# Performance work log

Hardware: AMD Instinct MI355X
Metric: run time of the kernel (lower is better)

## Reference

```python
import jax, jax.numpy as jnp
import numpy as np

NUM_HEADS = 8
TOP_K = 2
ROUTER_EPS = 1e-5
LN_EPS = 1e-5
ROPE_BASE = 10000.0


def _layernorm(x, g, b):
    m = x.mean(-1, keepdims=True)
    v = ((x - m) ** 2).mean(-1, keepdims=True)
    return (x - m) * jax.lax.rsqrt(v + LN_EPS) * g + b


def _rope_tables(frames, height, width, head_dim, dtype):
    # dim split per axis; head_dim divisible by 3 with even parts (96 -> 32/32/32)
    dpa = head_dim // 3

    def freqs(n, d):
        inv = 1.0 / (ROPE_BASE ** (jnp.arange(0, d, 2, dtype=jnp.float32) / d))
        f = jnp.outer(jnp.arange(n, dtype=jnp.float32), inv)
        return jnp.concatenate([f, f], axis=-1)  # [n, d]

    fx, fy, ft = freqs(width, dpa), freqs(height, dpa), freqs(frames, dpa)

    def grid(ax, ay, at):
        gx = jnp.broadcast_to(ax[None, None, :, :], (frames, height, width, dpa))
        gy = jnp.broadcast_to(ay[None, :, None, :], (frames, height, width, dpa))
        gt = jnp.broadcast_to(at[:, None, None, :], (frames, height, width, dpa))
        return jnp.concatenate([gx, gy, gt], -1).reshape(frames * height * width, 3 * dpa)

    cos = grid(jnp.cos(fx), jnp.cos(fy), jnp.cos(ft)).astype(dtype)
    sin = grid(jnp.sin(fx), jnp.sin(fy), jnp.sin(ft)).astype(dtype)
    return cos, sin


def _apply_rope(x, cos, sin):
    # x: [B, H, S, hd]; cos/sin: [S, hd] (broadcast over B, H)
    h = x.shape[-1] // 2
    rot = jnp.concatenate([-x[..., h:], x[..., :h]], axis=-1)
    return x * cos + rot * sin


def _expert(x, g, u, d):
    # SwiGLU expert: down(silu(gate(x)) * up(x))
    return (jax.nn.silu(x @ g) * (x @ u)) @ d


def _block(x, cos, sin, ln1_g, ln1_b, w_qkv, w_out, gate_w,
           eg, eu, ed, sg, su, sd, ln2_g, ln2_b):
    B, S, D = x.shape
    hd = D // NUM_HEADS
    # --- 3D-RoPE attention (pre-LN, non-causal) ---
    xn = _layernorm(x, ln1_g, ln1_b)
    qkv = (xn @ w_qkv).reshape(B, S, 3, NUM_HEADS, hd)
    q = jnp.moveaxis(qkv[:, :, 0], 1, 2)  # [B, H, S, hd]
    k = jnp.moveaxis(qkv[:, :, 1], 1, 2)
    v = jnp.moveaxis(qkv[:, :, 2], 1, 2)
    q = _apply_rope(q, cos, sin)
    k = _apply_rope(k, cos, sin)
    scores = jnp.einsum('bhqd,bhkd->bhqk', q, k) * (hd ** -0.5)
    attn = jax.nn.softmax(scores, axis=-1)
    o = jnp.einsum('bhqk,bhkd->bhqd', attn, v)
    o = jnp.moveaxis(o, 1, 2).reshape(B, S, D) @ w_out
    x = x + o
    # --- temporal MoE (top-k routing + shared expert) ---
    xf = x.reshape(-1, D)
    probs = jax.nn.softmax(xf @ gate_w, axis=-1)
    topv, topi = jax.lax.top_k(probs, TOP_K)
    topv = topv / (topv.sum(-1, keepdims=True) + ROUTER_EPS)
    E = eg.shape[0]
    # combine weight per (token, expert): sum over k slots routed to that expert
    comb = jnp.sum(topv[..., None] * (topi[..., None] == jnp.arange(E)), axis=1)  # [N, E]
    out = _expert(xf, sg, su, sd)  # shared expert on all tokens
    for e in range(E):
        out = out + comb[:, e:e + 1] * _expert(xf, eg[e], eu[e], ed[e])
    return _layernorm(x + out.reshape(B, S, D), ln2_g, ln2_b)


def setup_inputs() -> dict:
    key = jax.random.key(0)
    ks = jax.random.split(key, 10)
    B, S, D, F, E, L = 2, 2048, 768, 3072, 4, 2
    s = 0.02
    return {
        'x': jax.random.normal(ks[0], (B, S, D), jnp.float32),
        'height': 16, 'width': 16, 'frames': 8,
        'ln1_g': jnp.ones((L, D), jnp.float32),
        'ln1_b': jnp.zeros((L, D), jnp.float32),
        'w_qkv': jax.random.normal(ks[1], (L, D, 3 * D), jnp.float32) * s,
        'w_out': jax.random.normal(ks[2], (L, D, D), jnp.float32) * s,
        'gate_w': jax.random.normal(ks[3], (L, D, E), jnp.float32) * 0.01,
        'eg': jax.random.normal(ks[4], (L, E, D, F), jnp.float32) * s,
        'eu': jax.random.normal(ks[5], (L, E, D, F), jnp.float32) * s,
        'ed': jax.random.normal(ks[6], (L, E, F, D), jnp.float32) * s,
        'sg': jax.random.normal(ks[7], (L, D, F), jnp.float32) * s,
        'su': jax.random.normal(ks[8], (L, D, F), jnp.float32) * s,
        'sd': jax.random.normal(ks[9], (L, F, D), jnp.float32) * s,
        'ln2_g': jnp.ones((L, D), jnp.float32),
        'ln2_b': jnp.zeros((L, D), jnp.float32),
    }


def reference(x, height, width, frames, ln1_g, ln1_b, w_qkv, w_out, gate_w,
              eg, eu, ed, sg, su, sd, ln2_g, ln2_b):
    hd = x.shape[-1] // NUM_HEADS
    cos, sin = _rope_tables(frames, height, width, hd, x.dtype)
    for i in range(ln1_g.shape[0]):
        x = _block(x, cos, sin, ln1_g[i], ln1_b[i], w_qkv[i], w_out[i], gate_w[i],
                   eg[i], eu[i], ed[i], sg[i], su[i], sd[i], ln2_g[i], ln2_b[i])
    return x
```

## Files before the change

kernel.cpp:

```cpp
#include <hip/hip_runtime.h>
#include <stdint.h>

#define S_LEN 2048
#define DM    768
#define NHEAD 8
#define HDIM  96
#define HDP   128
#define FF    3072
#define FF2   6144
#define NEXP  4
#define NTOK  4096
#define NBH   16
#define HBROWS (2 * NTOK)

typedef unsigned short u16;
typedef short bf16x8 __attribute__((ext_vector_type(8)));
typedef float f32x4 __attribute__((ext_vector_type(4)));
typedef __attribute__((address_space(1))) void* gptr_t;
typedef __attribute__((address_space(3))) void* lptr_t;

__device__ __forceinline__ u16 f2bf(float f) {
  union { float f; uint32_t u; } v; v.f = f;
  uint32_t r = v.u + 0x7FFFu + ((v.u >> 16) & 1u);
  return (u16)(r >> 16);
}
__device__ __forceinline__ float bf2f(u16 h) {
  union { uint32_t u; float f; } v; v.u = ((uint32_t)h) << 16;
  return v.f;
}
__device__ __forceinline__ void split2(float f, u16& hi, u16& lo) {
  u16 h = f2bf(f);
  lo = f2bf(f - bf2f(h));
  hi = h;
}
__device__ __forceinline__ float siluf(float g) {
  return g / (1.0f + expf(-g));
}
__device__ __forceinline__ void gload16(const void* g, void* l) {
  __builtin_amdgcn_global_load_lds((gptr_t)(void*)g, (lptr_t)l, 16, 0, 0);
}

template<int MODE>
__global__ __launch_bounds__(256) void gemm_nt(
    const u16* __restrict__ A, const u16* __restrict__ B, void* __restrict__ Cv,
    int M, int N, int K, int lda, int ldb, long sA, long sB, long sC, int kspl,
    u16* __restrict__ hb)
{
  __shared__ u16 As[2][128 * 32];
  __shared__ u16 Bs[2][128 * 32];
  const int z = blockIdx.z;
  const int bh = z / kspl;
  const int kc = z - bh * kspl;
  const u16* Az = A + (long)bh * sA;
  const u16* Bz = B + (long)bh * sB;
  const int brow = blockIdx.y << 7;
  const int bcol = blockIdx.x << 7;
  const int tid = threadIdx.x;
  const int wid = tid >> 6;
  const int lane = tid & 63;
  const int wr = (wid >> 1) << 6;
  const int wc = (wid & 1) << 6;

  f32x4 acc[4][4] = {};
  const int a0 = (wid << 11) + (lane << 4);

  auto stage = [&](int buf, int k0) {
#pragma unroll
    for (int c = 0; c < 2; ++c) {
      int ab = a0 + (c << 10);
      int row = ab >> 6;
      int kcol = (ab & 63) >> 1;
      int ld = (wid << 11) + (c << 10);
      gload16(Az + (long)(brow + row) * lda + (k0 + kcol), (char*)As[buf] + ld);
      gload16(Bz + (long)(bcol + row) * ldb + (k0 + kcol), (char*)Bs[buf] + ld);
    }
  };

  const int kt = K / kspl;
  const int kbeg = kc * kt;
  const int nt = kt >> 5;
  stage(0, kbeg);
  __syncthreads();
  for (int t = 0; t < nt; ++t) {
    const int cur = t & 1;
    if (t + 1 < nt) stage(cur ^ 1, kbeg + ((t + 1) << 5));
    bf16x8 af[4], bfr[4];
    const int lr = lane & 15;
    const int lk = (lane >> 4) << 4;
#pragma unroll
    for (int m = 0; m < 4; ++m)
      af[m] = *(const bf16x8*)((const char*)As[cur] + (((wr + m * 16 + lr) << 6) + lk));
#pragma unroll
    for (int n = 0; n < 4; ++n)
      bfr[n] = *(const bf16x8*)((const char*)Bs[cur] + (((wc + n * 16 + lr) << 6) + lk));
#pragma unroll
    for (int m = 0; m < 4; ++m)
#pragma unroll
      for (int n = 0; n < 4; ++n)
        acc[m][n] = __builtin_amdgcn_mfma_f32_16x16x32_bf16(af[m], bfr[n], acc[m][n], 0, 0, 0);
    if (t + 1 < nt) __syncthreads();
  }

  const int crow0 = brow + wr + ((lane >> 4) << 2);
  const int ccol0 = bcol + wc + (lane & 15);
  const long cbase = (long)bh * sC;
  if constexpr (MODE == 5) {
    const int pbase = (bcol + wc) >> 5;
#pragma unroll
    for (int m = 0; m < 4; ++m)
#pragma unroll
      for (int np = 0; np < 2; ++np)
#pragma unroll
        for (int j = 0; j < 4; ++j) {
          int r = crow0 + m * 16 + j;
          float g = acc[m][2 * np][j], u = acc[m][2 * np + 1][j];
          int hcol = ((pbase + np) << 4) + (lane & 15);
          hb[(long)r * FF + hcol] = f2bf(siluf(g) * u);
        }
  } else {
#pragma unroll
    for (int m = 0; m < 4; ++m)
#pragma unroll
      for (int n = 0; n < 4; ++n)
#pragma unroll
        for (int j = 0; j < 4; ++j) {
          long idx = cbase + (long)(crow0 + m * 16 + j) * N + (ccol0 + n * 16);
          float v = acc[m][n][j];
          if constexpr (MODE == 2) ((u16*)Cv)[idx] = f2bf(v);
          else if constexpr (MODE == 3) unsafeAtomicAdd((float*)Cv + idx, v);
          else ((float*)Cv)[idx] = v;
        }
  }
}

template<int MODE>
__global__ __launch_bounds__(256) void gemm3_nt(
    const u16* __restrict__ Ah, const u16* __restrict__ Al,
    const u16* __restrict__ Bh, const u16* __restrict__ Bl,
    float* __restrict__ C,
    int M, int N, int K, int lda, int ldb, long sA, long sB, long sC, int kspl,
    u16* __restrict__ hbh, u16* __restrict__ hbl)
{
  __shared__ u16 Ash[2][128 * 32], Asl[2][128 * 32];
  __shared__ u16 Bsh[2][128 * 32], Bsl[2][128 * 32];
  const int z = blockIdx.z;
  const int bh = z / kspl;
  const int kc = z - bh * kspl;
  const u16* Azh = Ah + (long)bh * sA;
  const u16* Azl = Al + (long)bh * sA;
  const u16* Bzh = Bh + (long)bh * sB;
  const u16* Bzl = Bl + (long)bh * sB;
  const int brow = blockIdx.y << 7;
  const int bcol = blockIdx.x << 7;
  const int tid = threadIdx.x;
  const int wid = tid >> 6;
  const int lane = tid & 63;
  const int wr = (wid >> 1) << 6;
  const int wc = (wid & 1) << 6;

  f32x4 acc[4][4] = {};
  const int a0 = (wid << 11) + (lane << 4);

  auto stage = [&](int buf, int k0) {
#pragma unroll
    for (int c = 0; c < 2; ++c) {
      int ab = a0 + (c << 10);
      int row = ab >> 6;
      int kcol = (ab & 63) >> 1;
      long ao = (long)(brow + row) * lda + (k0 + kcol);
      long bo = (long)(bcol + row) * ldb + (k0 + kcol);
      int ld = (wid << 11) + (c << 10);
      gload16(Azh + ao, (char*)Ash[buf] + ld);
      gload16(Azl + ao, (char*)Asl[buf] + ld);
      gload16(Bzh + bo, (char*)Bsh[buf] + ld);
      gload16(Bzl + bo, (char*)Bsl[buf] + ld);
    }
  };

  const int kt = K / kspl;
  const int kbeg = kc * kt;
  const int nt = kt >> 5;
  stage(0, kbeg);
  __syncthreads();
  for (int t = 0; t < nt; ++t) {
    const int cur = t & 1;
    if (t + 1 < nt) stage(cur ^ 1, kbeg + ((t + 1) << 5));
    const int lr = lane & 15;
    const int lk = (lane >> 4) << 4;
    bf16x8 ah[4], al[4], bh_[4], bl[4];
#pragma unroll
    for (int m = 0; m < 4; ++m) {
      int off = ((wr + m * 16 + lr) << 6) + lk;
      ah[m] = *(const bf16x8*)((const char*)Ash[cur] + off);
      al[m] = *(const bf16x8*)((const char*)Asl[cur] + off);
    }
#pragma unroll
    for (int n = 0; n < 4; ++n) {
      int off = ((wc + n * 16 + lr) << 6) + lk;
      bh_[n] = *(const bf16x8*)((const char*)Bsh[cur] + off);
      bl[n] = *(const bf16x8*)((const char*)Bsl[cur] + off);
    }
#pragma unroll
    for (int m = 0; m < 4; ++m)
#pragma unroll
      for (int n = 0; n < 4; ++n) {
        acc[m][n] = __builtin_amdgcn_mfma_f32_16x16x32_bf16(al[m], bh_[n], acc[m][n], 0, 0, 0);
        acc[m][n] = __builtin_amdgcn_mfma_f32_16x16x32_bf16(ah[m], bl[n], acc[m][n], 0, 0, 0);
        acc[m][n] = __builtin_amdgcn_mfma_f32_16x16x32_bf16(ah[m], bh_[n], acc[m][n], 0, 0, 0);
      }
    if (t + 1 < nt) __syncthreads();
  }

  const int crow0 = brow + wr + ((lane >> 4) << 2);
  const int ccol0 = bcol + wc + (lane & 15);
  const long cbase = (long)bh * sC;
  if constexpr (MODE == 5) {
    const int pbase = (bcol + wc) >> 5;
#pragma unroll
    for (int m = 0; m < 4; ++m)
#pragma unroll
      for (int np = 0; np < 2; ++np)
#pragma unroll
        for (int j = 0; j < 4; ++j) {
          int r = crow0 + m * 16 + j;
          float g = acc[m][2 * np][j], u = acc[m][2 * np + 1][j];
          float h = siluf(g) * u;
          int hcol = ((pbase + np) << 4) + (lane & 15);
          u16 hh, ll; split2(h, hh, ll);
          hbh[(long)r * FF + hcol] = hh;
          hbl[(long)r * FF + hcol] = ll;
        }
  } else {
#pragma unroll
    for (int m = 0; m < 4; ++m)
#pragma unroll
      for (int n = 0; n < 4; ++n)
#pragma unroll
        for (int j = 0; j < 4; ++j) {
          long idx = cbase + (long)(crow0 + m * 16 + j) * N + (ccol0 + n * 16);
          if constexpr (MODE == 3) unsafeAtomicAdd(&C[idx], acc[m][n][j]);
          else C[idx] = acc[m][n][j];
        }
  }
}

template<int MODE>
__global__ __launch_bounds__(256) void gemm3i_nt(
    const u16* __restrict__ Ah, const u16* __restrict__ Al,
    const u16* __restrict__ Bh, const u16* __restrict__ Bl,
    float* __restrict__ C, int N, int K, int lda, int ldb, int ldc,
    const int* __restrict__ perm, const int* __restrict__ cnt,
    const int* __restrict__ cbase, int kspl, long wstride,
    u16* __restrict__ hbh, u16* __restrict__ hbl, const float* __restrict__ comb)
{
  const int z = blockIdx.z;
  const int e = z / kspl;
  const int kc = z - e * kspl;
  const int cn = cnt[e];
  const int brow = blockIdx.y << 7;
  if (brow >= cn) return;
  const int cb = cbase[e];
  const int* pe = perm + e * NTOK;
  const u16* Bhe = Bh + (long)e * wstride;
  const u16* Ble = Bl + (long)e * wstride;
  __shared__ u16 Ash[2][128 * 32], Asl[2][128 * 32];
  __shared__ u16 Bsh[2][128 * 32], Bsl[2][128 * 32];
  const int bcol = blockIdx.x << 7;
  const int tid = threadIdx.x;
  const int wid = tid >> 6;
  const int lane = tid & 63;
  const int wr = (wid >> 1) << 6;
  const int wc = (wid & 1) << 6;

  f32x4 acc[4][4] = {};
  const int a0 = (wid << 11) + (lane << 4);

  int arow[2];
#pragma unroll
  for (int c = 0; c < 2; ++c) {
    int ab = a0 + (c << 10);
    int row = ab >> 6;
    int g = brow + row;
    if constexpr (MODE == 5) {
      arow[c] = (g < cn) ? pe[g] : pe[brow];
    } else {
      arow[c] = cb + ((g < cn) ? g : (cn - 1));
    }
  }

  auto stage = [&](int buf, int k0) {
#pragma unroll
    for (int c = 0; c < 2; ++c) {
      int ab = a0 + (c << 10);
      int row = ab >> 6;
      int kcol = (ab & 63) >> 1;
      int ld = (wid << 11) + (c << 10);
      gload16(Ah + (long)arow[c] * lda + (k0 + kcol), (char*)Ash[buf] + ld);
      gload16(Al + (long)arow[c] * lda + (k0 + kcol), (char*)Asl[buf] + ld);
      long bo = (long)(bcol + row) * ldb + (k0 + kcol);
      gload16(Bhe + bo, (char*)Bsh[buf] + ld);
      gload16(Ble + bo, (char*)Bsl[buf] + ld);
    }
  };

  const int kt = K / kspl;
  const int kbeg = kc * kt;
  const int nt = kt >> 5;
  stage(0, kbeg);
  __syncthreads();
  for (int t = 0; t < nt; ++t) {
    const int cur = t & 1;
    if (t + 1 < nt) stage(cur ^ 1, kbeg + ((t + 1) << 5));
    const int lr = lane & 15;
    const int lk = (lane >> 4) << 4;
    bf16x8 ah[4], al[4], bh_[4], bl[4];
#pragma unroll
    for (int m = 0; m < 4; ++m) {
      int off = ((wr + m * 16 + lr) << 6) + lk;
      ah[m] = *(const bf16x8*)((const char*)Ash[cur] + off);
      al[m] = *(const bf16x8*)((const char*)Asl[cur] + off);
    }
#pragma unroll
    for (int n = 0; n < 4; ++n) {
      int off = ((wc + n * 16 + lr) << 6) + lk;
      bh_[n] = *(const bf16x8*)((const char*)Bsh[cur] + off);
      bl[n] = *(const bf16x8*)((const char*)Bsl[cur] + off);
    }
#pragma unroll
    for (int m = 0; m < 4; ++m)
#pragma unroll
      for (int n = 0; n < 4; ++n) {
        acc[m][n] = __builtin_amdgcn_mfma_f32_16x16x32_bf16(al[m], bh_[n], acc[m][n], 0, 0, 0);
        acc[m][n] = __builtin_amdgcn_mfma_f32_16x16x32_bf16(ah[m], bl[n], acc[m][n], 0, 0, 0);
        acc[m][n] = __builtin_amdgcn_mfma_f32_16x16x32_bf16(ah[m], bh_[n], acc[m][n], 0, 0, 0);
      }
    if (t + 1 < nt) __syncthreads();
  }

  const int crow0 = brow + wr + ((lane >> 4) << 2);
  const int ccol0 = bcol + wc + (lane & 15);
  if constexpr (MODE == 5) {
    const int pbase = (bcol + wc) >> 5;
#pragma unroll
    for (int m = 0; m < 4; ++m)
#pragma unroll
      for (int j = 0; j < 4; ++j) {
        int r = crow0 + m * 16 + j;
        if (r < cn) {
          float w = comb[pe[r] * 4 + e];
#pragma unroll
          for (int np = 0; np < 2; ++np) {
            float g = acc[m][2 * np][j], u = acc[m][2 * np + 1][j];
            float h = siluf(g) * u * w;
            int hcol = ((pbase + np) << 4) + (lane & 15);
            u16 hh, ll; split2(h, hh, ll);
            hbh[(long)(cb + r) * FF + hcol] = hh;
            hbl[(long)(cb + r) * FF + hcol] = ll;
          }
        }
      }
  } else {
#pragma unroll
    for (int m = 0; m < 4; ++m)
#pragma unroll
      for (int n = 0; n < 4; ++n)
#pragma unroll
        for (int j = 0; j < 4; ++j) {
          int r = crow0 + m * 16 + j;
          if (r < cn) {
            int col = ccol0 + n * 16;
            unsafeAtomicAdd(&C[(long)pe[r] * ldc + col], acc[m][n][j]);
          }
        }
  }
}

template<int MODE>
__global__ __launch_bounds__(256) void gemmi_nt(
    const u16* __restrict__ A, const u16* __restrict__ B, void* __restrict__ Cv,
    int N, int K, int lda, int ldb, int ldc,
    const int* __restrict__ perm, const int* __restrict__ cnt,
    const int* __restrict__ cbase, int kspl, long wstride,
    u16* __restrict__ hb, const float* __restrict__ comb)
{
  const int z = blockIdx.z;
  const int e = z / kspl;
  const int kc = z - e * kspl;
  const int cn = cnt[e];
  const int brow = blockIdx.y << 7;
  if (brow >= cn) return;
  const int cb = cbase[e];
  const int* pe = perm + e * NTOK;
  const u16* Be = B + (long)e * wstride;
  __shared__ u16 As[2][128 * 32];
  __shared__ u16 Bs[2][128 * 32];
  const int bcol = blockIdx.x << 7;
  const int tid = threadIdx.x;
  const int wid = tid >> 6;
  const int lane = tid & 63;
  const int wr = (wid >> 1) << 6;
  const int wc = (wid & 1) << 6;

  f32x4 acc[4][4] = {};
  const int a0 = (wid << 11) + (lane << 4);

  int arow[2];
#pragma unroll
  for (int c = 0; c < 2; ++c) {
    int ab = a0 + (c << 10);
    int row = ab >> 6;
    int g = brow + row;
    if constexpr (MODE == 5) {
      arow[c] = (g < cn) ? pe[g] : pe[brow];
    } else {
      arow[c] = cb + ((g < cn) ? g : (cn - 1));
    }
  }

  auto stage = [&](int buf, int k0) {
#pragma unroll
    for (int c = 0; c < 2; ++c) {
      int ab = a0 + (c << 10);
      int row = ab >> 6;
      int kcol = (ab & 63) >> 1;
      int ld = (wid << 11) + (c << 10);
      gload16(A + (long)arow[c] * lda + (k0 + kcol), (char*)As[buf] + ld);
      gload16(Be + (long)(bcol + row) * ldb + (k0 + kcol), (char*)Bs[buf] + ld);
    }
  };

  const int kt = K / kspl;
  const int kbeg = kc * kt;
  const int nt = kt >> 5;
  stage(0, kbeg);
  __syncthreads();
  for (int t = 0; t < nt; ++t) {
    const int cur = t & 1;
    if (t + 1 < nt) stage(cur ^ 1, kbeg + ((t + 1) << 5));
    bf16x8 af[4], bfr[4];
    const int lr = lane & 15;
    const int lk = (lane >> 4) << 4;
#pragma unroll
    for (int m = 0; m < 4; ++m)
      af[m] = *(const bf16x8*)((const char*)As[cur] + (((wr + m * 16 + lr) << 6) + lk));
#pragma unroll
    for (int n = 0; n < 4; ++n)
      bfr[n] = *(const bf16x8*)((const char*)Bs[cur] + (((wc + n * 16 + lr) << 6) + lk));
#pragma unroll
    for (int m = 0; m < 4; ++m)
#pragma unroll
      for (int n = 0; n < 4; ++n)
        acc[m][n] = __builtin_amdgcn_mfma_f32_16x16x32_bf16(af[m], bfr[n], acc[m][n], 0, 0, 0);
    if (t + 1 < nt) __syncthreads();
  }

  const int crow0 = brow + wr + ((lane >> 4) << 2);
  const int ccol0 = bcol + wc + (lane & 15);
  if constexpr (MODE == 5) {
    const int pbase = (bcol + wc) >> 5;
#pragma unroll
    for (int m = 0; m < 4; ++m)
#pragma unroll
      for (int j = 0; j < 4; ++j) {
        int r = crow0 + m * 16 + j;
        if (r < cn) {
          float w = comb[pe[r] * 4 + e];
#pragma unroll
          for (int np = 0; np < 2; ++np) {
            float g = acc[m][2 * np][j], u = acc[m][2 * np + 1][j];
            int hcol = ((pbase + np) << 4) + (lane & 15);
            hb[(long)(cb + r) * FF + hcol] = f2bf(siluf(g) * u * w);
          }
        }
      }
  } else {
#pragma unroll
    for (int m = 0; m < 4; ++m)
#pragma unroll
      for (int n = 0; n < 4; ++n)
#pragma unroll
        for (int j = 0; j < 4; ++j) {
          int r = crow0 + m * 16 + j;
          if (r < cn) {
            int col = ccol0 + n * 16;
            unsafeAtomicAdd((float*)Cv + (long)pe[r] * ldc + col, acc[m][n][j]);
          }
        }
  }
}

__global__ __launch_bounds__(256, 2) void fattn_k(
    const u16* __restrict__ qh, const u16* __restrict__ ql,
    const u16* __restrict__ kh, const u16* __restrict__ kl,
    const u16* __restrict__ vth, const u16* __restrict__ vtl,
    u16* __restrict__ omh, u16* __restrict__ oml, float scale)
{
  __shared__ u16 Ksh[64 * 128], Ksl[64 * 128];
  __shared__ u16 Vsh[128 * 64], Vsl[128 * 64];
  const int bh = blockIdx.x;
  const int qt = blockIdx.y;
  const int tid = threadIdx.x, wid = tid >> 6, lane = tid & 63;
  const int lr = lane & 15, lg = lane >> 4;
  const int q0 = qt * 64 + wid * 16;
  const long bhoff = (long)bh * S_LEN * HDP;
  const u16* Qh = qh + bhoff;  const u16* Ql = ql + bhoff;
  const u16* Kgh = kh + bhoff; const u16* Kgl = kl + bhoff;
  const u16* Vgh = vth + bhoff; const u16* Vgl = vtl + bhoff;

  bf16x8 qfh[4], qfl[4];
#pragma unroll
  for (int kk = 0; kk < 4; ++kk) {
    long o = (long)(q0 + lr) * HDP + kk * 32 + lg * 8;
    qfh[kk] = *(const bf16x8*)(Qh + o);
    qfl[kk] = *(const bf16x8*)(Ql + o);
  }

  f32x4 oacc[6] = {};
  float rm[4], rls[4];
#pragma unroll
  for (int j = 0; j < 4; ++j) { rm[j] = -1e30f; rls[j] = 0.f; }

  for (int t = 0; t < S_LEN / 64; ++t) {
    __syncthreads();
#pragma unroll
    for (int c = 0; c < 4; ++c) {
      int off = (tid + (c << 8)) << 4;
      {
        int lb = off ^ ((((off >> 8) & 7)) << 4);
        int row = lb >> 8, colh = (lb & 255) >> 1;
        long src = (long)(t * 64 + row) * HDP + colh;
        gload16(Kgh + src, (char*)Ksh + off);
        gload16(Kgl + src, (char*)Ksl + off);
      }
      {
        int lb = off ^ ((((off >> 7) & 7)) << 4);
        int row = lb >> 7, colh = (lb & 127) >> 1;
        long src = (long)row * S_LEN + t * 64 + colh;
        gload16(Vgh + src, (char*)Vsh + off);
        gload16(Vgl + src, (char*)Vsl + off);
      }
    }
    __syncthreads();

    f32x4 sacc[4] = {};
#pragma unroll
    for (int kk = 0; kk < 4; ++kk) {
      bf16x8 kbh[4], kbl[4];
#pragma unroll
      for (int n = 0; n < 4; ++n) {
        int byte = ((n * 16 + lr) << 8) + (kk << 6) + (lg << 4);
        byte ^= ((byte >> 8) & 7) << 4;
        kbh[n] = *(const bf16x8*)((const char*)Ksh + byte);
        kbl[n] = *(const bf16x8*)((const char*)Ksl + byte);
      }
      __builtin_amdgcn_s_setprio(1);
#pragma unroll
      for (int n = 0; n < 4; ++n) {
        sacc[n] = __builtin_amdgcn_mfma_f32_16x16x32_bf16(qfl[kk], kbh[n], sacc[n], 0, 0, 0);
        sacc[n] = __builtin_amdgcn_mfma_f32_16x16x32_bf16(qfh[kk], kbl[n], sacc[n], 0, 0, 0);
        sacc[n] = __builtin_amdgcn_mfma_f32_16x16x32_bf16(qfh[kk], kbh[n], sacc[n], 0, 0, 0);
      }
      __builtin_amdgcn_s_setprio(0);
    }
    __syncthreads();

#pragma unroll
    for (int j = 0; j < 4; ++j) {
      float mx = fmaxf(fmaxf(sacc[0][j], sacc[1][j]),
                       fmaxf(sacc[2][j], sacc[3][j])) * scale;
      mx = fmaxf(mx, __shfl_xor(mx, 1));
      mx = fmaxf(mx, __shfl_xor(mx, 2));
      mx = fmaxf(mx, __shfl_xor(mx, 4));
      mx = fmaxf(mx, __shfl_xor(mx, 8));
      float mnew = fmaxf(rm[j], mx);
      float corr = __expf(rm[j] - mnew);
      rm[j] = mnew;
      float ps = 0.f;
#pragma unroll
      for (int n = 0; n < 4; ++n) {
        float p = __expf(sacc[n][j] * scale - mnew);
        sacc[n][j] = p; ps += p;
      }
      ps += __shfl_xor(ps, 1); ps += __shfl_xor(ps, 2);
      ps += __shfl_xor(ps, 4); ps += __shfl_xor(ps, 8);
      rls[j] = rls[j] * corr + ps;
#pragma unroll
      for (int n2 = 0; n2 < 6; ++n2) oacc[n2][j] *= corr;
    }

    char* Pwh = (char*)Ksh + (wid << 11);
    char* Pwl = (char*)Ksl + (wid << 11);
#pragma unroll
    for (int n = 0; n < 4; ++n)
#pragma unroll
      for (int j = 0; j < 4; ++j) {
        int row = lg * 4 + j;
        int byte = (row << 7) + ((n * 16 + lr) << 1);
        byte ^= ((byte >> 7) & 7) << 4;
        u16 h, l; split2(sacc[n][j], h, l);
        *(u16*)(Pwh + byte) = h;
        *(u16*)(Pwl + byte) = l;
      }
    bf16x8 pah[2], pal[2];
#pragma unroll
    for (int kk = 0; kk < 2; ++kk) {
      int byte = (lr << 7) + (kk << 6) + (lg << 4);
      byte ^= ((byte >> 7) & 7) << 4;
      pah[kk] = *(const bf16x8*)(Pwh + byte);
      pal[kk] = *(const bf16x8*)(Pwl + byte);
    }

#pragma unroll
    for (int kk = 0; kk < 2; ++kk) {
      bf16x8 vbh[6], vbl[6];
#pragma unroll
      for (int n2 = 0; n2 < 6; ++n2) {
        int byte = ((n2 * 16 + lr) << 7) + (kk << 6) + (lg << 4);
        byte ^= ((byte >> 7) & 7) << 4;
        vbh[n2] = *(const bf16x8*)((const char*)Vsh + byte);
        vbl[n2] = *(const bf16x8*)((const char*)Vsl + byte);
      }
      __builtin_amdgcn_s_setprio(1);
#pragma unroll
      for (int n2 = 0; n2 < 6; ++n2) {
        oacc[n2] = __builtin_amdgcn_mfma_f32_16x16x32_bf16(pal[kk], vbh[n2], oacc[n2], 0, 0, 0);
        oacc[n2] = __builtin_amdgcn_mfma_f32_16x16x32_bf16(pah[kk], vbl[n2], oacc[n2], 0, 0, 0);
        oacc[n2] = __builtin_amdgcn_mfma_f32_16x16x32_bf16(pah[kk], vbh[n2], oacc[n2], 0, 0, 0);
      }
      __builtin_amdgcn_s_setprio(0);
    }
  }

  const int b = bh >> 3, h = bh & 7;
#pragma unroll
  for (int j = 0; j < 4; ++j) {
    float inv = 1.0f / rls[j];
    int q = q0 + lg * 4 + j;
    long base = ((long)(b * S_LEN + q)) * DM + h * HDIM;
#pragma unroll
    for (int n2 = 0; n2 < 6; ++n2) {
      int d = n2 * 16 + lr;
      u16 hh, ll; split2(oacc[n2][j] * inv, hh, ll);
      omh[base + d] = hh; oml[base + d] = ll;
    }
  }
}

__global__ void wconv_t(const float* __restrict__ in, u16* __restrict__ outh,
                        u16* __restrict__ outl, int R, int C, int ilv,
                        long inStride, long outStride) {
  __shared__ float tile[32][33];
  long z = blockIdx.z;
  in += z * inStride; outh += z * outStride; outl += z * outStride;
  int c0 = blockIdx.x << 5, r0 = blockIdx.y << 5;
  int tx = threadIdx.x;
  for (int rr = threadIdx.y; rr < 32; rr += 8)
    tile[rr][tx] = in[(long)(r0 + rr) * C + (c0 + tx)];
  __syncthreads();
  for (int rr = threadIdx.y; rr < 32; rr += 8) {
    u16 h, l; split2(tile[tx][rr], h, l);
    int f = c0 + rr;
    long orow = (ilv < 0) ? f : (((f >> 4) << 5) + (ilv << 4) + (f & 15));
    long o = orow * R + (r0 + tx);
    outh[o] = h; outl[o] = l;
  }
}

__global__ __launch_bounds__(256) void ln_k(const float* __restrict__ in,
    const float* __restrict__ g, const float* __restrict__ b,
    float* __restrict__ outf, u16* __restrict__ outh, u16* __restrict__ outl) {
  int row = blockIdx.x;
  const float* x = in + (long)row * DM;
  int tid = threadIdx.x;
  float v[3], s = 0.f, ss = 0.f;
#pragma unroll
  for (int i = 0; i < 3; ++i) { v[i] = x[tid + (i << 8)]; s += v[i]; ss += v[i] * v[i]; }
  __shared__ float red[2][4];
  for (int o = 32; o; o >>= 1) { s += __shfl_down(s, o); ss += __shfl_down(ss, o); }
  int wid = tid >> 6, lane = tid & 63;
  if (!lane) { red[0][wid] = s; red[1][wid] = ss; }
  __syncthreads();
  s = red[0][0] + red[0][1] + red[0][2] + red[0][3];
  ss = red[1][0] + red[1][1] + red[1][2] + red[1][3];
  float mean = s * (1.f / DM);
  float var = ss * (1.f / DM) - mean * mean;
  float rs = rsqrtf(var + 1e-5f);
#pragma unroll
  for (int i = 0; i < 3; ++i) {
    int c = tid + (i << 8);
    float y = (v[i] - mean) * rs * g[c] + b[c];
    if (outf) outf[(long)row * DM + c] = y;
    if (outh) { u16 h, l; split2(y, h, l); outh[(long)row * DM + c] = h; outl[(long)row * DM + c] = l; }
  }
}

__global__ void rope_tables_k(float* __restrict__ cosT, float* __restrict__ sinT) {
  int s = blockIdx.x, d = threadIdx.x;
  int xc = s & 15, y = (s >> 4) & 15, t = s >> 8;
  int axis = d / 32, fi = d & 15;
  int coord = axis == 0 ? xc : (axis == 1 ? y : t);
  float inv = powf(10000.0f, -(float)fi / 16.0f);
  float ang = (float)coord * inv;
  cosT[s * HDIM + d] = cosf(ang);
  sinT[s * HDIM + d] = sinf(ang);
}

__global__ __launch_bounds__(256) void rope_apply_k(const float* __restrict__ qkv,
    const float* __restrict__ cosT, const float* __restrict__ sinT,
    u16* __restrict__ qh, u16* __restrict__ ql,
    u16* __restrict__ kh, u16* __restrict__ kl) {
  int bs = blockIdx.x;
  int b = bs >> 11, s = bs & 2047;
  const float* base = qkv + ((long)(b * S_LEN + s) * 3) * DM;
  for (int idx = threadIdx.x; idx < DM; idx += 256) {
    int h = idx / HDIM, d = idx - h * HDIM;
    float c = cosT[s * HDIM + d], sn = sinT[s * HDIM + d];
    int pair = (d < 48) ? idx + 48 : idx - 48;
    float qv = base[idx], kv = base[DM + idx];
    float qr = (d < 48) ? -base[pair] : base[pair];
    float kr = (d < 48) ? -base[DM + pair] : base[DM + pair];
    long o = ((long)(b * NHEAD + h) * S_LEN + s) * HDP + d;
    u16 hh, ll;
    split2(qv * c + qr * sn, hh, ll); qh[o] = hh; ql[o] = ll;
    split2(kv * c + kr * sn, hh, ll); kh[o] = hh; kl[o] = ll;
  }
  int t = threadIdx.x;
  int h = t >> 5, d = HDIM + (t & 31);
  long o = ((long)(b * NHEAD + h) * S_LEN + s) * HDP + d;
  qh[o] = 0; ql[o] = 0; kh[o] = 0; kl[o] = 0;
}

__global__ void v_transpose_k(const float* __restrict__ qkv,
                              u16* __restrict__ vh, u16* __restrict__ vl) {
  __shared__ float tile[32][33];
  int bh = blockIdx.z, b = bh >> 3, h = bh & 7;
  int s0 = blockIdx.x << 5, d0 = blockIdx.y << 5;
  int tx = threadIdx.x;
  for (int r = threadIdx.y; r < 32; r += 8) {
    int s = s0 + r, d = d0 + tx;
    float v = 0.f;
    if (d < HDIM) v = qkv[((long)(b * S_LEN + s) * 3 + 2) * DM + h * HDIM + d];
    tile[r][tx] = v;
  }
  __syncthreads();
  for (int r = threadIdx.y; r < 32; r += 8) {
    int d = d0 + r;
    u16 hh, ll; split2(tile[tx][r], hh, ll);
    long o = ((long)bh * HDP + d) * S_LEN + (s0 + tx);
    vh[o] = hh; vl[o] = ll;
  }
}

__global__ __launch_bounds__(256) void router_k(const float* __restrict__ x,
    const float* __restrict__ gw, float* __restrict__ comb, int* __restrict__ mask) {
  int tok = blockIdx.x * 4 + (threadIdx.x >> 6);
  int lane = threadIdx.x & 63;
  const float* xr = x + (long)tok * DM;
  float a0 = 0, a1 = 0, a2 = 0, a3 = 0;
  for (int i = lane; i < DM; i += 64) {
    float xv = xr[i];
    const float* g = gw + i * 4;
    a0 += xv * g[0]; a1 += xv * g[1]; a2 += xv * g[2]; a3 += xv * g[3];
  }
  for (int o = 32; o; o >>= 1) {
    a0 += __shfl_down(a0, o); a1 += __shfl_down(a1, o);
    a2 += __shfl_down(a2, o); a3 += __shfl_down(a3, o);
  }
  if (lane == 0) {
    float p[4] = {a0, a1, a2, a3};
    float mx = fmaxf(fmaxf(p[0], p[1]), fmaxf(p[2], p[3]));
    float s = 0.f;
    for (int e = 0; e < 4; ++e) { p[e] = expf(p[e] - mx); s += p[e]; }
    for (int e = 0; e < 4; ++e) p[e] /= s;
    int i1 = 0;
    for (int e = 1; e < 4; ++e) if (p[e] > p[i1]) i1 = e;
    int i2 = -1;
    for (int e = 0; e < 4; ++e) if (e != i1 && (i2 < 0 || p[e] > p[i2])) i2 = e;
    float ssum = p[i1] + p[i2] + 1e-5f;
    float out[4] = {0, 0, 0, 0};
    out[i1] = p[i1] / ssum; out[i2] = p[i2] / ssum;
    for (int e = 0; e < 4; ++e) comb[tok * 4 + e] = out[e];
    mask[tok] = (1 << i1) | (1 << i2);
  }
}

__global__ void scan_k(const int* __restrict__ mask, int* __restrict__ perm,
                       int* __restrict__ cnt) {
  __shared__ int sd[256];
  __shared__ int base;
  int tid = threadIdx.x;
  int e = blockIdx.x;
  if (tid == 0) base = 0;
  __syncthreads();
  for (int c = 0; c < NTOK / 256; ++c) {
    int tok = c * 256 + tid;
    int f = (mask[tok] >> e) & 1;
    sd[tid] = f;
    __syncthreads();
    for (int s = 1; s < 256; s <<= 1) {
      int v = (tid >= s) ? sd[tid - s] : 0;
      __syncthreads();
      sd[tid] += v;
      __syncthreads();
    }
    if (f) perm[e * NTOK + base + sd[tid] - 1] = tok;
    int tot = sd[255];
    __syncthreads();
    if (tid == 0) base += tot;
    __syncthreads();
  }
  if (tid == 0) cnt[e] = base;
}

__global__ void cbase_k(const int* __restrict__ cnt, int* __restrict__ cbase) {
  if (threadIdx.x == 0) {
    int b = 0;
    for (int e = 0; e < NEXP; ++e) { cbase[e] = b; b += cnt[e]; }
  }
}

__global__ void f2b_k(const float* __restrict__ src, u16* __restrict__ dst, long n) {
  long i = (long)blockIdx.x * 256 + threadIdx.x;
  if (i < n) dst[i] = f2bf(src[i]);
}

__global__ void f2bsplit_k(const float* __restrict__ src, u16* __restrict__ dh,
                           u16* __restrict__ dl, long n) {
  long i = (long)blockIdx.x * 256 + threadIdx.x;
  if (i < n) { u16 h, l; split2(src[i], h, l); dh[i] = h; dl[i] = l; }
}

extern "C" void kernel_launch(void* const* d_in, const int* in_sizes, int n_in,
                              void* d_out, int out_size, void* d_ws, size_t ws_size,
                              hipStream_t stream) {
  (void)in_sizes; (void)n_in; (void)out_size; (void)ws_size;
  const float* x_in  = (const float*)d_in[0];
  const float* ln1_g = (const float*)d_in[4];
  const float* ln1_b = (const float*)d_in[5];
  const float* w_qkv = (const float*)d_in[6];
  const float* w_out = (const float*)d_in[7];
  const float* gatew = (const float*)d_in[8];
  const float* eg    = (const float*)d_in[9];
  const float* eu    = (const float*)d_in[10];
  const float* ed    = (const float*)d_in[11];
  const float* sg    = (const float*)d_in[12];
  const float* su    = (const float*)d_in[13];
  const float* sd    = (const float*)d_in[14];
  const float* ln2_g = (const float*)d_in[15];
  const float* ln2_b = (const float*)d_in[16];

  float* xc = (float*)d_out;
  char* W = (char*)d_ws;
  size_t off = 0;
  auto alloc = [&](size_t bytes) {
    size_t o = off; off = (off + bytes + 255) & ~(size_t)255; return o;
  };
  size_t o_cos  = alloc((size_t)S_LEN * HDIM * 4);
  size_t o_sin  = alloc((size_t)S_LEN * HDIM * 4);
  size_t o_xnh  = alloc((size_t)NTOK * DM * 2);
  size_t o_xnl  = alloc((size_t)NTOK * DM * 2);
  size_t o_comb = alloc((size_t)NTOK * 4 * 4);
  size_t o_mask = alloc((size_t)NTOK * 4);
  size_t o_perm = alloc((size_t)NEXP * NTOK * 4);
  size_t o_cnt  = alloc(256);
  size_t o_cb   = alloc(256);
  const size_t EGU_B = (size_t)NEXP * FF2 * DM * 2;
  const size_t SGU_B = (size_t)FF2 * DM * 2;
  const size_t SD_B  = (size_t)DM * FF * 2;
  const size_t A_BYTES = 2 * EGU_B + 2 * SGU_B + 2 * SD_B;
  size_t oA = alloc(A_BYTES);
  size_t o_qkv = oA;
  size_t o_qph = oA + (size_t)NTOK * 3 * DM * 4;
  size_t o_qpl = o_qph + (size_t)NBH * S_LEN * HDP * 2;
  size_t o_kph = o_qpl + (size_t)NBH * S_LEN * HDP * 2;
  size_t o_kpl = o_kph + (size_t)NBH * S_LEN * HDP * 2;
  size_t o_vth = o_kpl + (size_t)NBH * S_LEN * HDP * 2;
  size_t o_vtl = o_vth + (size_t)NBH * HDP * S_LEN * 2;
  size_t o_omh = o_vtl + (size_t)NBH * HDP * S_LEN * 2;
  size_t o_oml = o_omh + (size_t)NTOK * DM * 2;
  size_t o_eguh = oA;
  size_t o_egul = oA + EGU_B;
  size_t o_sguh = oA + 2 * EGU_B;
  size_t o_sgul = o_sguh + SGU_B;
  size_t o_sdh  = o_sgul + SGU_B;
  size_t o_sdl  = o_sdh + SD_B;
  size_t o_edh  = oA;
  size_t o_edl  = oA + (size_t)NEXP * DM * FF * 2;
  const size_t H_BYTES = (size_t)2 * HBROWS * FF * 2;
  size_t oH = alloc(H_BYTES);
  size_t o_wqh = oH;
  size_t o_wql = o_wqh + (size_t)3 * DM * DM * 2;
  size_t o_woh = o_wql + (size_t)3 * DM * DM * 2;
  size_t o_wol = o_woh + (size_t)DM * DM * 2;
  size_t o_hbh = oH;
  size_t o_hbl = oH + (size_t)HBROWS * FF * 2;

  float* cosT = (float*)(W + o_cos);
  float* sinT = (float*)(W + o_sin);
  u16*   xnh  = (u16*)(W + o_xnh);
  u16*   xnl  = (u16*)(W + o_xnl);
  float* comb = (float*)(W + o_comb);
  int* maskb  = (int*)(W + o_mask);
  int* permb  = (int*)(W + o_perm);
  int* cntb   = (int*)(W + o_cnt);
  int* cbaseb = (int*)(W + o_cb);
  float* qkv  = (float*)(W + o_qkv);
  u16 *qph = (u16*)(W + o_qph), *qpl = (u16*)(W + o_qpl);
  u16 *kph = (u16*)(W + o_kph), *kpl = (u16*)(W + o_kpl);
  u16 *vth = (u16*)(W + o_vth), *vtl = (u16*)(W + o_vtl);
  u16 *omh = (u16*)(W + o_omh), *oml = (u16*)(W + o_oml);
  u16 *eguh = (u16*)(W + o_eguh), *egul = (u16*)(W + o_egul);
  u16 *sguh = (u16*)(W + o_sguh), *sgul = (u16*)(W + o_sgul);
  u16 *sdh = (u16*)(W + o_sdh), *sdl = (u16*)(W + o_sdl);
  u16 *edh = (u16*)(W + o_edh), *edl = (u16*)(W + o_edl);
  u16 *wqh = (u16*)(W + o_wqh), *wql = (u16*)(W + o_wql);
  u16 *woh = (u16*)(W + o_woh), *wol = (u16*)(W + o_wol);
  u16 *hbh = (u16*)(W + o_hbh), *hbl = (u16*)(W + o_hbl);

  const long ND = (long)NTOK * DM;
  const int gND = (int)((ND + 255) / 256);

  hipMemcpyAsync(xc, x_in, (size_t)ND * 4, hipMemcpyDeviceToDevice, stream);
  rope_tables_k<<<S_LEN, HDIM, 0, stream>>>(cosT, sinT);

  dim3 tb(32, 8, 1);
  for (int l = 0; l < 2; ++l) {
    const float* wqkv_l = w_qkv + (size_t)l * DM * 3 * DM;
    const float* wout_l = w_out + (size_t)l * DM * DM;
    const float* gw_l   = gatew + (size_t)l * DM * 4;
    const float* eg_l = eg + (size_t)l * NEXP * DM * FF;
    const float* eu_l = eu + (size_t)l * NEXP * DM * FF;
    const float* ed_l = ed + (size_t)l * NEXP * FF * DM;
    const float* sg_l = sg + (size_t)l * DM * FF;
    const float* su_l = su + (size_t)l * DM * FF;
    const float* sd_l = sd + (size_t)l * FF * DM;

    wconv_t<<<dim3(3 * DM / 32, DM / 32, 1), tb, 0, stream>>>(wqkv_l, wqh, wql, DM, 3 * DM, -1, 0, 0);
    wconv_t<<<dim3(DM / 32, DM / 32, 1), tb, 0, stream>>>(wout_l, woh, wol, DM, DM, -1, 0, 0);

    ln_k<<<NTOK, 256, 0, stream>>>(xc, ln1_g + l * DM, ln1_b + l * DM, nullptr, xnh, xnl);
    gemm3_nt<0><<<dim3(3 * DM >> 7, NTOK >> 7, 1), 256, 0, stream>>>(
        xnh, xnl, wqh, wql, qkv, NTOK, 3 * DM, DM, DM, DM, 0, 0, 0, 1, nullptr, nullptr);
    rope_apply_k<<<NTOK, 256, 0, stream>>>(qkv, cosT, sinT, qph, qpl, kph, kpl);
    v_transpose_k<<<dim3(S_LEN / 32, HDP / 32, NBH), tb, 0, stream>>>(qkv, vth, vtl);
    fattn_k<<<dim3(NBH, S_LEN / 64), dim3(256), 0, stream>>>(
        qph, qpl, kph, kpl, vth, vtl, omh, oml, 0.10206207261596575f);
    gemm3_nt<3><<<dim3(DM >> 7, NTOK >> 7, 2), 256, 0, stream>>>(
        omh, oml, woh, wol, xc, NTOK, DM, DM, DM, DM, 0, 0, 0, 2, nullptr, nullptr);

    router_k<<<NTOK / 4, 256, 0, stream>>>(xc, gw_l, comb, maskb);
    scan_k<<<NEXP, 256, 0, stream>>>(maskb, permb, cntb);
    cbase_k<<<1, 64, 0, stream>>>(cntb, cbaseb);

    wconv_t<<<dim3(FF / 32, DM / 32, 1), tb, 0, stream>>>(sg_l, sguh, sgul, DM, FF, 0, 0, 0);
    wconv_t<<<dim3(FF / 32, DM / 32, 1), tb, 0, stream>>>(su_l, sguh, sgul, DM, FF, 1, 0, 0);
    wconv_t<<<dim3(DM / 32, FF / 32, 1), tb, 0, stream>>>(sd_l, sdh, sdl, FF, DM, -1, 0, 0);
    wconv_t<<<dim3(FF / 32, DM / 32, NEXP), tb, 0, stream>>>(
        eg_l, eguh, egul, DM, FF, 0, (long)DM * FF, (long)FF2 * DM);
    wconv_t<<<dim3(FF / 32, DM / 32, NEXP), tb, 0, stream>>>(
        eu_l, eguh, egul, DM, FF, 1, (long)DM * FF, (long)FF2 * DM);

    if (l == 0) {
      f2bsplit_k<<<gND, 256, 0, stream>>>(xc, xnh, xnl, ND);
      gemm3_nt<5><<<dim3(FF2 >> 7, NTOK >> 7, 1), 256, 0, stream>>>(
          xnh, xnl, sguh, sgul, nullptr, NTOK, FF2, DM, DM, DM, 0, 0, 0, 1, hbh, hbl);
      gemm3_nt<3><<<dim3(DM >> 7, NTOK >> 7, 4), 256, 0, stream>>>(
          hbh, hbl, sdh, sdl, xc, NTOK, DM, FF, FF, FF, 0, 0, 0, 4, nullptr, nullptr);
      gemm3i_nt<5><<<dim3(FF2 >> 7, NTOK >> 7, NEXP), 256, 0, stream>>>(
          xnh, xnl, eguh, egul, nullptr, FF2, DM, DM, DM, FF2,
          permb, cntb, cbaseb, 1, (long)FF2 * DM, hbh, hbl, comb);
      wconv_t<<<dim3(DM / 32, FF / 32, NEXP), tb, 0, stream>>>(
          ed_l, edh, edl, FF, DM, -1, (long)FF * DM, (long)DM * FF);
      gemm3i_nt<1><<<dim3(DM >> 7, NTOK >> 7, NEXP * 2), 256, 0, stream>>>(
          hbh, hbl, edh, edl, xc, DM, FF, FF, FF, DM,
          permb, cntb, cbaseb, 2, (long)DM * FF, nullptr, nullptr, nullptr);
    } else {
      f2b_k<<<gND, 256, 0, stream>>>(xc, xnh, ND);
      gemm_nt<5><<<dim3(FF2 >> 7, NTOK >> 7, 1), 256, 0, stream>>>(
          xnh, sguh, nullptr, NTOK, FF2, DM, DM, DM, 0, 0, 0, 1, hbh);
      gemm_nt<3><<<dim3(DM >> 7, NTOK >> 7, 4), 256, 0, stream>>>(
          hbh, sdh, xc, NTOK, DM, FF, FF, FF, 0, 0, 0, 4, nullptr);
      gemmi_nt<5><<<dim3(FF2 >> 7, NTOK >> 7, NEXP), 256, 0, stream>>>(
          xnh, eguh, nullptr, FF2, DM, DM, DM, FF2,
          permb, cntb, cbaseb, 1, (long)FF2 * DM, hbh, comb);
      wconv_t<<<dim3(DM / 32, FF / 32, NEXP), tb, 0, stream>>>(
          ed_l, edh, edl, FF, DM, -1, (long)FF * DM, (long)DM * FF);
      gemmi_nt<3><<<dim3(DM >> 7, NTOK >> 7, NEXP * 2), 256, 0, stream>>>(
          hbh, edh, xc, DM, FF, FF, FF, DM,
          permb, cntb, cbaseb, 2, (long)DM * FF, nullptr, nullptr);
    }
    ln_k<<<NTOK, 256, 0, stream>>>(xc, ln2_g + l * DM, ln2_b + l * DM, xc, nullptr, nullptr);
  }
}
```

Baseline: 1.860 ms.

## Swizzle LDS tiles in GEMMs and skip low-half weight conversion outside layer 0

Applies an XOR swizzle to the LDS byte offsets used by all four GEMM kernels. The swizzle is applied to the global source column during staging and to the LDS read address, so MFMA fragment reads no longer hit the same banks. Separately, weight conversion for layers after the first writes only the bf16 high part, since those layers use single-precision-bf16 GEMMs, which cuts conversion stores. The swizzle must permute staging and reads consistently; an inconsistency would produce wrong results.

```diff
diff --git a/kernel.cpp b/kernel.cpp
--- a/kernel.cpp
+++ b/kernel.cpp
@@ -38,6 +38,9 @@
 }
 __device__ __forceinline__ void gload16(const void* g, void* l) {
   __builtin_amdgcn_global_load_lds((gptr_t)(void*)g, (lptr_t)l, 16, 0, 0);
+}
+__device__ __forceinline__ int swz(int byte) {
+  return byte ^ (((byte >> 7) & 3) << 4);
 }
 
 template<int MODE>
@@ -68,8 +71,9 @@
 #pragma unroll
     for (int c = 0; c < 2; ++c) {
       int ab = a0 + (c << 10);
+      int lb = swz(ab);
       int row = ab >> 6;
-      int kcol = (ab & 63) >> 1;
+      int kcol = (lb & 63) >> 1;
       int ld = (wid << 11) + (c << 10);
       gload16(Az + (long)(brow + row) * lda + (k0 + kcol), (char*)As[buf] + ld);
       gload16(Bz + (long)(bcol + row) * ldb + (k0 + kcol), (char*)Bs[buf] + ld);
@@ -89,10 +93,10 @@
     const int lk = (lane >> 4) << 4;
 #pragma unroll
     for (int m = 0; m < 4; ++m)
-      af[m] = *(const bf16x8*)((const char*)As[cur] + (((wr + m * 16 + lr) << 6) + lk));
+      af[m] = *(const bf16x8*)((const char*)As[cur] + swz((((wr + m * 16 + lr) << 6) + lk)));
 #pragma unroll
     for (int n = 0; n < 4; ++n)
-      bfr[n] = *(const bf16x8*)((const char*)Bs[cur] + (((wc + n * 16 + lr) << 6) + lk));
+      bfr[n] = *(const bf16x8*)((const char*)Bs[cur] + swz((((wc + n * 16 + lr) << 6) + lk)));
 #pragma unroll
     for (int m = 0; m < 4; ++m)
 #pragma unroll
@@ -165,8 +169,9 @@
 #pragma unroll
     for (int c = 0; c < 2; ++c) {
       int ab = a0 + (c << 10);
+      int lb = swz(ab);
       int row = ab >> 6;
-      int kcol = (ab & 63) >> 1;
+      int kcol = (lb & 63) >> 1;
       long ao = (long)(brow + row) * lda + (k0 + kcol);
       long bo = (long)(bcol + row) * ldb + (k0 + kcol);
       int ld = (wid << 11) + (c << 10);
@@ -190,13 +195,13 @@
     bf16x8 ah[4], al[4], bh_[4], bl[4];
 #pragma unroll
     for (int m = 0; m < 4; ++m) {
-      int off = ((wr + m * 16 + lr) << 6) + lk;
+      int off = swz(((wr + m * 16 + lr) << 6) + lk);
       ah[m] = *(const bf16x8*)((const char*)Ash[cur] + off);
       al[m] = *(const bf16x8*)((const char*)Asl[cur] + off);
     }
 #pragma unroll
     for (int n = 0; n < 4; ++n) {
-      int off = ((wc + n * 16 + lr) << 6) + lk;
+      int off = swz(((wc + n * 16 + lr) << 6) + lk);
       bh_[n] = *(const bf16x8*)((const char*)Bsh[cur] + off);
       bl[n] = *(const bf16x8*)((const char*)Bsl[cur] + off);
     }
@@ -292,8 +297,9 @@
 #pragma unroll
     for (int c = 0; c < 2; ++c) {
       int ab = a0 + (c << 10);
+      int lb = swz(ab);
       int row = ab >> 6;
-      int kcol = (ab & 63) >> 1;
+      int kcol = (lb & 63) >> 1;
       int ld = (wid << 11) + (c << 10);
       gload16(Ah + (long)arow[c] * lda + (k0 + kcol), (char*)Ash[buf] + ld);
       gload16(Al + (long)arow[c] * lda + (k0 + kcol), (char*)Asl[buf] + ld);
@@ -316,13 +322,13 @@
     bf16x8 ah[4], al[4], bh_[4], bl[4];
 #pragma unroll
     for (int m = 0; m < 4; ++m) {
-      int off = ((wr + m * 16 + lr) << 6) + lk;
+      int off = swz(((wr + m * 16 + lr) << 6) + lk);
       ah[m] = *(const bf16x8*)((const char*)Ash[cur] + off);
       al[m] = *(const bf16x8*)((const char*)Asl[cur] + off);
     }
 #pragma unroll
     for (int n = 0; n < 4; ++n) {
-      int off = ((wc + n * 16 + lr) << 6) + lk;
+      int off = swz(((wc + n * 16 + lr) << 6) + lk);
       bh_[n] = *(const bf16x8*)((const char*)Bsh[cur] + off);
       bl[n] = *(const bf16x8*)((const char*)Bsl[cur] + off);
     }
@@ -421,8 +427,9 @@
 #pragma unroll
     for (int c = 0; c < 2; ++c) {
       int ab = a0 + (c << 10);
+      int lb = swz(ab);
       int row = ab >> 6;
-      int kcol = (ab & 63) >> 1;
+      int kcol = (lb & 63) >> 1;
       int ld = (wid << 11) + (c << 10);
       gload16(A + (long)arow[c] * lda + (k0 + kcol), (char*)As[buf] + ld);
       gload16(Be + (long)(bcol + row) * ldb + (k0 + kcol), (char*)Bs[buf] + ld);
@@ -442,10 +449,10 @@
     const int lk = (lane >> 4) << 4;
 #pragma unroll
     for (int m = 0; m < 4; ++m)
-      af[m] = *(const bf16x8*)((const char*)As[cur] + (((wr + m * 16 + lr) << 6) + lk));
+      af[m] = *(const bf16x8*)((const char*)As[cur] + swz((((wr + m * 16 + lr) << 6) + lk)));
 #pragma unroll
     for (int n = 0; n < 4; ++n)
-      bfr[n] = *(const bf16x8*)((const char*)Bs[cur] + (((wc + n * 16 + lr) << 6) + lk));
+      bfr[n] = *(const bf16x8*)((const char*)Bs[cur] + swz((((wc + n * 16 + lr) << 6) + lk)));
 #pragma unroll
     for (int m = 0; m < 4; ++m)
 #pragma unroll
@@ -651,7 +658,8 @@
                         long inStride, long outStride) {
   __shared__ float tile[32][33];
   long z = blockIdx.z;
-  in += z * inStride; outh += z * outStride; outl += z * outStride;
+  in += z * inStride; outh += z * outStride;
+  if (outl) outl += z * outStride;
   int c0 = blockIdx.x << 5, r0 = blockIdx.y << 5;
   int tx = threadIdx.x;
   for (int rr = threadIdx.y; rr < 32; rr += 8)
@@ -662,7 +670,8 @@
     int f = c0 + rr;
     long orow = (ilv < 0) ? f : (((f >> 4) << 5) + (ilv << 4) + (f & 15));
     long o = orow * R + (r0 + tx);
-    outh[o] = h; outl[o] = l;
+    outh[o] = h;
+    if (outl) outl[o] = l;
   }
 }
 
@@ -952,15 +961,15 @@
     scan_k<<<NEXP, 256, 0, stream>>>(maskb, permb, cntb);
     cbase_k<<<1, 64, 0, stream>>>(cntb, cbaseb);
 
-    wconv_t<<<dim3(FF / 32, DM / 32, 1), tb, 0, stream>>>(sg_l, sguh, sgul, DM, FF, 0, 0, 0);
-    wconv_t<<<dim3(FF / 32, DM / 32, 1), tb, 0, stream>>>(su_l, sguh, sgul, DM, FF, 1, 0, 0);
-    wconv_t<<<dim3(DM / 32, FF / 32, 1), tb, 0, stream>>>(sd_l, sdh, sdl, FF, DM, -1, 0, 0);
-    wconv_t<<<dim3(FF / 32, DM / 32, NEXP), tb, 0, stream>>>(
-        eg_l, eguh, egul, DM, FF, 0, (long)DM * FF, (long)FF2 * DM);
-    wconv_t<<<dim3(FF / 32, DM / 32, NEXP), tb, 0, stream>>>(
-        eu_l, eguh, egul, DM, FF, 1, (long)DM * FF, (long)FF2 * DM);
-
     if (l == 0) {
+      wconv_t<<<dim3(FF / 32, DM / 32, 1), tb, 0, stream>>>(sg_l, sguh, sgul, DM, FF, 0, 0, 0);
+      wconv_t<<<dim3(FF / 32, DM / 32, 1), tb, 0, stream>>>(su_l, sguh, sgul, DM, FF, 1, 0, 0);
+      wconv_t<<<dim3(DM / 32, FF / 32, 1), tb, 0, stream>>>(sd_l, sdh, sdl, FF, DM, -1, 0, 0);
+      wconv_t<<<dim3(FF / 32, DM / 32, NEXP), tb, 0, stream>>>(
+          eg_l, eguh, egul, DM, FF, 0, (long)DM * FF, (long)FF2 * DM);
+      wconv_t<<<dim3(FF / 32, DM / 32, NEXP), tb, 0, stream>>>(
+          eu_l, eguh, egul, DM, FF, 1, (long)DM * FF, (long)FF2 * DM);
+
       f2bsplit_k<<<gND, 256, 0, stream>>>(xc, xnh, xnl, ND);
       gemm3_nt<5><<<dim3(FF2 >> 7, NTOK >> 7, 1), 256, 0, stream>>>(
           xnh, xnl, sguh, sgul, nullptr, NTOK, FF2, DM, DM, DM, 0, 0, 0, 1, hbh, hbl);
@@ -975,6 +984,14 @@
           hbh, hbl, edh, edl, xc, DM, FF, FF, FF, DM,
           permb, cntb, cbaseb, 2, (long)DM * FF, nullptr, nullptr, nullptr);
     } else {
+      wconv_t<<<dim3(FF / 32, DM / 32, 1), tb, 0, stream>>>(sg_l, sguh, nullptr, DM, FF, 0, 0, 0);
+      wconv_t<<<dim3(FF / 32, DM / 32, 1), tb, 0, stream>>>(su_l, sguh, nullptr, DM, FF, 1, 0, 0);
+      wconv_t<<<dim3(DM / 32, FF / 32, 1), tb, 0, stream>>>(sd_l, sdh, nullptr, FF, DM, -1, 0, 0);
+      wconv_t<<<dim3(FF / 32, DM / 32, NEXP), tb, 0, stream>>>(
+          eg_l, eguh, nullptr, DM, FF, 0, (long)DM * FF, (long)FF2 * DM);
+      wconv_t<<<dim3(FF / 32, DM / 32, NEXP), tb, 0, stream>>>(
+          eu_l, eguh, nullptr, DM, FF, 1, (long)DM * FF, (long)FF2 * DM);
+
       f2b_k<<<gND, 256, 0, stream>>>(xc, xnh, ND);
       gemm_nt<5><<<dim3(FF2 >> 7, NTOK >> 7, 1), 256, 0, stream>>>(
           xnh, sguh, nullptr, NTOK, FF2, DM, DM, DM, 0, 0, 0, 1, hbh);
@@ -984,7 +1001,7 @@
           xnh, eguh, nullptr, FF2, DM, DM, DM, FF2,
           permb, cntb, cbaseb, 1, (long)FF2 * DM, hbh, comb);
       wconv_t<<<dim3(DM / 32, FF / 32, NEXP), tb, 0, stream>>>(
-          ed_l, edh, edl, FF, DM, -1, (long)FF * DM, (long)DM * FF);
+          ed_l, edh, nullptr, FF, DM, -1, (long)FF * DM, (long)DM * FF);
       gemmi_nt<3><<<dim3(DM >> 7, NTOK >> 7, NEXP * 2), 256, 0, stream>>>(
           hbh, edh, xc, DM, FF, FF, FF, DM,
           permb, cntb, cbaseb, 2, (long)DM * FF, nullptr, nullptr);
```

Measured after the change: 1.850 ms. Within noise of the previous version (-0.6%).
